# Performance work log

Measured on AMD Instinct MI355X. Metric: run time of the kernel, lower is better.

## Reference

```python
import jax, jax.numpy as jnp
import numpy as np

N_NODES = 50000
N_EDGES = 800000
F_IN = 128
F_OUT = 128


def gcn_conv(x, W, b, src, tgt, w, n):
    # x: [n, F_in]; GCNConv with add_self_loops=True, improved=False (fill=1.0)
    lin = x @ W  # [n, F_out]
    deg = jax.ops.segment_sum(w, tgt, num_segments=n) + 1.0  # self-loop weight 1
    dinv = jax.lax.rsqrt(deg)
    normw = dinv[src] * w * dinv[tgt]  # [E]
    agg = jax.ops.segment_sum(lin[src] * normw[:, None], tgt, num_segments=n)
    return agg + lin * (dinv * dinv)[:, None] + b


def setup_inputs() -> dict:
    key = jax.random.key(0)
    ks = jax.random.split(key, 16)
    X = jax.random.normal(ks[0], (1, N_NODES, F_IN), jnp.float32)
    edge_index = jax.random.randint(ks[1], (2, N_EDGES), 0, N_NODES, jnp.int64)
    edge_weight = jax.random.uniform(ks[2], (N_EDGES,), jnp.float32)
    H = jax.random.normal(ks[3], (1, N_NODES, F_OUT), jnp.float32)
    s = 1.0 / np.sqrt(F_IN)
    s2 = 1.0 / np.sqrt(2 * F_OUT)
    params = {
        'W_z': jax.random.uniform(ks[4], (F_IN, F_OUT), jnp.float32, -s, s),
        'b_z': jnp.zeros((F_OUT,), jnp.float32),
        'W_r': jax.random.uniform(ks[5], (F_IN, F_OUT), jnp.float32, -s, s),
        'b_r': jnp.zeros((F_OUT,), jnp.float32),
        'W_h': jax.random.uniform(ks[6], (F_IN, F_OUT), jnp.float32, -s, s),
        'b_h': jnp.zeros((F_OUT,), jnp.float32),
        'Wl_z': jax.random.uniform(ks[7], (2 * F_OUT, F_OUT), jnp.float32, -s2, s2),
        'bl_z': jax.random.uniform(ks[8], (F_OUT,), jnp.float32, -s2, s2),
        'Wl_r': jax.random.uniform(ks[9], (2 * F_OUT, F_OUT), jnp.float32, -s2, s2),
        'bl_r': jax.random.uniform(ks[10], (F_OUT,), jnp.float32, -s2, s2),
        'Wl_h': jax.random.uniform(ks[11], (2 * F_OUT, F_OUT), jnp.float32, -s2, s2),
        'bl_h': jax.random.uniform(ks[12], (F_OUT,), jnp.float32, -s2, s2),
    }
    return dict(X=X, edge_index=edge_index, edge_weight=edge_weight, H=H, **params)


def reference(X, edge_index, edge_weight, H,
              W_z, b_z, W_r, b_r, W_h, b_h,
              Wl_z, bl_z, Wl_r, bl_r, Wl_h, bl_h):
    B, N, _ = X.shape
    n = B * N
    x = X.reshape(n, -1)
    src, tgt = edge_index[0], edge_index[1]

    cz = gcn_conv(x, W_z, b_z, src, tgt, edge_weight, n).reshape(B, N, -1)
    Z = jax.nn.sigmoid(jnp.concatenate([cz, H], axis=2) @ Wl_z + bl_z)

    cr = gcn_conv(x, W_r, b_r, src, tgt, edge_weight, n).reshape(B, N, -1)
    R = jax.nn.sigmoid(jnp.concatenate([cr, H], axis=2) @ Wl_r + bl_r)

    ch = gcn_conv(x, W_h, b_h, src, tgt, edge_weight, n).reshape(B, N, -1)
    H_tilde = jnp.tanh(jnp.concatenate([ch, H * R], axis=2) @ Wl_h + bl_h)

    return Z * H + (1.0 - Z) * H_tilde
```

## Files before the change

### kernel.cpp

```cpp
#include <hip/hip_runtime.h>
#include <hip/hip_bf16.h>

#define N_NODES 50000
#define N_EDGES 800000
#define M_PAD   50048
#define NBLK5   1564
#define CAP     96

typedef __attribute__((ext_vector_type(8))) short bf16x8_t;
typedef __attribute__((ext_vector_type(4))) float f32x4_t;

__device__ __forceinline__ unsigned short f2bf(float f) {
    unsigned u = __float_as_uint(f);
    u += 0x7FFFu + ((u >> 16) & 1u);
    return (unsigned short)(u >> 16);
}
__device__ __forceinline__ float bf2f(unsigned short h) {
    return __uint_as_float(((unsigned)h) << 16);
}


__global__ void prep1_kernel(const float* __restrict__ Wz, const float* __restrict__ Wr,
                             const float* __restrict__ Wh,
                             const float* __restrict__ bz, const float* __restrict__ br,
                             const float* __restrict__ bh,
                             const float* __restrict__ Wlz, const float* __restrict__ Wlr,
                             const float* __restrict__ Wlh,
                             const float* __restrict__ blz, const float* __restrict__ blr,
                             const float* __restrict__ blh,
                             float* __restrict__ Pf, float* __restrict__ cg,
                             int* __restrict__ counts) {
    int tid = blockIdx.x * 256 + threadIdx.x;
    if (tid < N_NODES) counts[tid] = 0;
    if (tid < 3 * 16384) {
        int g = tid / 16384, k = (tid / 128) % 128, n = tid & 127;
        const float* W  = (g == 0) ? Wz  : (g == 1) ? Wr  : Wh;
        const float* Wl = (g == 0) ? Wlz : (g == 1) ? Wlr : Wlh;
        float acc = 0.f;
        #pragma unroll 8
        for (int j = 0; j < 128; ++j)
            acc = fmaf(W[k * 128 + j], Wl[j * 128 + n], acc);
        Pf[tid] = acc;
    } else if (tid < 3 * 16384 + 384) {
        int u = tid - 3 * 16384;
        int g = u / 128, n = u & 127;
        const float* b  = (g == 0) ? bz  : (g == 1) ? br  : bh;
        const float* Wl = (g == 0) ? Wlz : (g == 1) ? Wlr : Wlh;
        const float* bl = (g == 0) ? blz : (g == 1) ? blr : blh;
        float acc = bl[n];
        #pragma unroll 8
        for (int j = 0; j < 128; ++j)
            acc = fmaf(b[j], Wl[j * 128 + n], acc);
        cg[u] = acc;
    }
}

__global__ void wfrag2_kernel(const float* __restrict__ Pf,
                              const float* __restrict__ Wlz, const float* __restrict__ Wlr,
                              const float* __restrict__ Wlh,
                              unsigned short* __restrict__ Wf2) {
    int tid = blockIdx.x * 256 + threadIdx.x;
    if (tid >= 6 * 2048) return;
    int m = tid / 2048, t = tid % 2048;
    int nt = t / 256, ks = (t / 64) % 4, lane = t % 64;
    const float* src;
    if (m < 3) src = Pf + m * 16384;
    else       src = ((m == 3) ? Wlz : (m == 4) ? Wlr : Wlh) + 128 * 128;
    unsigned short* dst = Wf2 + m * 16384 + ((nt * 4 + ks) * 64 + lane) * 8;
    int n = nt * 16 + (lane & 15);
    int k0 = ks * 32 + 8 * (lane >> 4);
    #pragma unroll
    for (int j = 0; j < 8; ++j) dst[j] = f2bf(src[(k0 + j) * 128 + n]);
}

__global__ void place_kernel(const int* __restrict__ EI, const float* __restrict__ EW,
                             int* __restrict__ counts, int2* __restrict__ rec,
                             const float* __restrict__ Hf, unsigned short* __restrict__ Hb) {
    int i = blockIdx.x * 256 + threadIdx.x;
    if (i < N_NODES * 32) {
        float4 h = ((const float4*)Hf)[i];
        ushort4 b;
        b.x = f2bf(h.x); b.y = f2bf(h.y); b.z = f2bf(h.z); b.w = f2bf(h.w);
        ((ushort4*)Hb)[i] = b;
    }
    if (i < N_EDGES) {
        int s = EI[i];
        int t = EI[N_EDGES + i];
        int pos = atomicAdd(&counts[t], 1);
        if (pos < CAP) rec[(size_t)t * CAP + pos] = make_int2(s, __float_as_int(EW[i]));
    }
}

__global__ void deg_kernel(const int* __restrict__ counts, const int2* __restrict__ rec,
                           float* __restrict__ dinv) {
    int n = blockIdx.x * 256 + threadIdx.x;
    if (n >= N_NODES) return;
    int c = counts[n]; c = (c < CAP) ? c : CAP;
    const int2* rb = rec + (size_t)n * CAP;
    float d = 1.0f;
    #pragma unroll 4
    for (int e = 0; e < c; ++e) d += __int_as_float(rb[e].y);
    dinv[n] = rsqrtf(d);
}

__global__ void convert_kernel(const float* __restrict__ X, const float* __restrict__ dinv,
                               unsigned short* __restrict__ Xb) {
    int i = blockIdx.x * 256 + threadIdx.x;
    if (i >= N_NODES * 32) return;
    int node = i >> 5;
    float di = dinv[node];
    float4 x = ((const float4*)X)[i];
    ushort4 a;
    a.x = f2bf(di * x.x); a.y = f2bf(di * x.y); a.z = f2bf(di * x.z); a.w = f2bf(di * x.w);
    ((ushort4*)Xb)[i] = a;
}


__global__ __launch_bounds__(512) void fused_kernel(const unsigned short* __restrict__ Xb,
                                                    const unsigned short* __restrict__ Hb,
                                                    const float* __restrict__ dinv,
                                                    const int* __restrict__ counts,
                                                    const int2* __restrict__ rec,
                                                    const unsigned short* __restrict__ Wf2,
                                                    const float* __restrict__ cg,
                                                    float* __restrict__ out) {
    __shared__ unsigned short ys[32][136];
    __shared__ unsigned short hs[32][136];
    __shared__ unsigned short rls[32][136];
    int tid = threadIdx.x;
    int wave = tid >> 6, lane = tid & 63;
    int rowbase = blockIdx.x * 32;
    int rlo = lane & 15;
    int kg = 8 * (lane >> 4);
    int n0 = wave;

    {
        int r = tid >> 4, co = (tid & 15) * 8;
        int row = rowbase + r;
        bf16x8_t h;
        if (row < N_NODES) h = *(const bf16x8_t*)(Hb + (size_t)row * 128 + co);
        else {
            #pragma unroll
            for (int j = 0; j < 8; ++j) h[j] = 0;
        }
        *(bf16x8_t*)(&hs[r][co]) = h;
    }

    {
        int nl = wave * 4 + (lane >> 4);
        int half = (lane >> 3) & 1;
        int lg = lane & 7;
        int node = rowbase + nl;
        float acc[16];
        #pragma unroll
        for (int j = 0; j < 16; ++j) acc[j] = 0.f;
        if (node < N_NODES) {
            if (half == 0) {
                bf16x8_t x0 = *(const bf16x8_t*)(Xb + (size_t)node * 128 + lg * 16);
                bf16x8_t x1 = *(const bf16x8_t*)(Xb + (size_t)node * 128 + lg * 16 + 8);
                #pragma unroll
                for (int j = 0; j < 8; ++j) {
                    acc[j] = bf2f((unsigned short)x0[j]);
                    acc[8 + j] = bf2f((unsigned short)x1[j]);
                }
            }
            int c = counts[node]; c = (c < CAP) ? c : CAP;
            const int2* rb = rec + (size_t)node * CAP;
            int e = half;
            int2 r;
            bf16x8_t xa0, xa1;
            float wcur = 0.f;
            if (e < c) {
                r = rb[e];
                xa0 = *(const bf16x8_t*)(Xb + (size_t)r.x * 128 + lg * 16);
                xa1 = *(const bf16x8_t*)(Xb + (size_t)r.x * 128 + lg * 16 + 8);
                wcur = __int_as_float(r.y);
                if (e + 2 < c) r = rb[e + 2];
            }
            while (e < c) {
                bf16x8_t xb0, xb1;
                float wn = 0.f;
                int en = e + 2;
                if (en < c) {
                    xb0 = *(const bf16x8_t*)(Xb + (size_t)r.x * 128 + lg * 16);
                    xb1 = *(const bf16x8_t*)(Xb + (size_t)r.x * 128 + lg * 16 + 8);
                    wn = __int_as_float(r.y);
                    if (en + 2 < c) r = rb[en + 2];
                }
                #pragma unroll
                for (int j = 0; j < 8; ++j) {
                    acc[j] = fmaf(wcur, bf2f((unsigned short)xa0[j]), acc[j]);
                    acc[8 + j] = fmaf(wcur, bf2f((unsigned short)xa1[j]), acc[8 + j]);
                }
                xa0 = xb0; xa1 = xb1; wcur = wn;
                e = en;
            }
        }
        #pragma unroll
        for (int j = 0; j < 16; ++j) acc[j] += __shfl_xor(acc[j], 8, 64);
        if (half == 0) {
            float dt = (node < N_NODES) ? dinv[node] : 0.f;
            ushort4 o0, o1, o2, o3;
            o0.x = f2bf(dt * acc[0]);  o0.y = f2bf(dt * acc[1]);
            o0.z = f2bf(dt * acc[2]);  o0.w = f2bf(dt * acc[3]);
            o1.x = f2bf(dt * acc[4]);  o1.y = f2bf(dt * acc[5]);
            o1.z = f2bf(dt * acc[6]);  o1.w = f2bf(dt * acc[7]);
            o2.x = f2bf(dt * acc[8]);  o2.y = f2bf(dt * acc[9]);
            o2.z = f2bf(dt * acc[10]); o2.w = f2bf(dt * acc[11]);
            o3.x = f2bf(dt * acc[12]); o3.y = f2bf(dt * acc[13]);
            o3.z = f2bf(dt * acc[14]); o3.w = f2bf(dt * acc[15]);
            *(ushort4*)(&ys[nl][lg * 16])      = o0;
            *(ushort4*)(&ys[nl][lg * 16 + 4])  = o1;
            *(ushort4*)(&ys[nl][lg * 16 + 8])  = o2;
            *(ushort4*)(&ys[nl][lg * 16 + 12]) = o3;
        }
    }
    __syncthreads();

    const unsigned short* Az = Wf2;
    const unsigned short* Ar = Wf2 + 16384;
    const unsigned short* Ah = Wf2 + 2 * 16384;
    const unsigned short* Bz = Wf2 + 3 * 16384;
    const unsigned short* Br = Wf2 + 4 * 16384;
    const unsigned short* Bh = Wf2 + 5 * 16384;
    int col = n0 * 16 + rlo;

    {
        f32x4_t a0 = f32x4_t{0.f, 0.f, 0.f, 0.f};
        f32x4_t a1 = f32x4_t{0.f, 0.f, 0.f, 0.f};
        #pragma unroll
        for (int ks = 0; ks < 4; ++ks) {
            bf16x8_t y0 = *(const bf16x8_t*)(&ys[rlo][ks * 32 + kg]);
            bf16x8_t y1 = *(const bf16x8_t*)(&ys[16 + rlo][ks * 32 + kg]);
            bf16x8_t b = *(const bf16x8_t*)(Ar + ((n0 * 4 + ks) * 64 + lane) * 8);
            a0 = __builtin_amdgcn_mfma_f32_16x16x32_bf16(y0, b, a0, 0, 0, 0);
            a1 = __builtin_amdgcn_mfma_f32_16x16x32_bf16(y1, b, a1, 0, 0, 0);
        }
        #pragma unroll
        for (int ks = 0; ks < 4; ++ks) {
            bf16x8_t h0 = *(const bf16x8_t*)(&hs[rlo][ks * 32 + kg]);
            bf16x8_t h1 = *(const bf16x8_t*)(&hs[16 + rlo][ks * 32 + kg]);
            bf16x8_t b = *(const bf16x8_t*)(Br + ((n0 * 4 + ks) * 64 + lane) * 8);
            a0 = __builtin_amdgcn_mfma_f32_16x16x32_bf16(h0, b, a0, 0, 0, 0);
            a1 = __builtin_amdgcn_mfma_f32_16x16x32_bf16(h1, b, a1, 0, 0, 0);
        }
        float crv = cg[128 + col];
        #pragma unroll
        for (int r = 0; r < 4; ++r) {
            float p0 = a0[r] + crv;
            float p1 = a1[r] + crv;
            rls[4 * (lane >> 4) + r][col] = f2bf(1.0f / (1.0f + __expf(-p0)));
            rls[16 + 4 * (lane >> 4) + r][col] = f2bf(1.0f / (1.0f + __expf(-p1)));
        }
    }
    __syncthreads();

    {
        f32x4_t az0 = f32x4_t{0.f, 0.f, 0.f, 0.f};
        f32x4_t az1 = f32x4_t{0.f, 0.f, 0.f, 0.f};
        f32x4_t at0 = f32x4_t{0.f, 0.f, 0.f, 0.f};
        f32x4_t at1 = f32x4_t{0.f, 0.f, 0.f, 0.f};
        #pragma unroll
        for (int ks = 0; ks < 4; ++ks) {
            bf16x8_t y0 = *(const bf16x8_t*)(&ys[rlo][ks * 32 + kg]);
            bf16x8_t y1 = *(const bf16x8_t*)(&ys[16 + rlo][ks * 32 + kg]);
            bf16x8_t bz_ = *(const bf16x8_t*)(Az + ((n0 * 4 + ks) * 64 + lane) * 8);
            bf16x8_t bh_ = *(const bf16x8_t*)(Ah + ((n0 * 4 + ks) * 64 + lane) * 8);
            az0 = __builtin_amdgcn_mfma_f32_16x16x32_bf16(y0, bz_, az0, 0, 0, 0);
            az1 = __builtin_amdgcn_mfma_f32_16x16x32_bf16(y1, bz_, az1, 0, 0, 0);
            at0 = __builtin_amdgcn_mfma_f32_16x16x32_bf16(y0, bh_, at0, 0, 0, 0);
            at1 = __builtin_amdgcn_mfma_f32_16x16x32_bf16(y1, bh_, at1, 0, 0, 0);
        }
        #pragma unroll
        for (int ks = 0; ks < 4; ++ks) {
            bf16x8_t h0 = *(const bf16x8_t*)(&hs[rlo][ks * 32 + kg]);
            bf16x8_t h1 = *(const bf16x8_t*)(&hs[16 + rlo][ks * 32 + kg]);
            bf16x8_t rf0 = *(const bf16x8_t*)(&rls[rlo][ks * 32 + kg]);
            bf16x8_t rf1 = *(const bf16x8_t*)(&rls[16 + rlo][ks * 32 + kg]);
            bf16x8_t hr0, hr1;
            #pragma unroll
            for (int j = 0; j < 8; ++j) {
                hr0[j] = (short)f2bf(bf2f((unsigned short)h0[j]) * bf2f((unsigned short)rf0[j]));
                hr1[j] = (short)f2bf(bf2f((unsigned short)h1[j]) * bf2f((unsigned short)rf1[j]));
            }
            bf16x8_t bz_ = *(const bf16x8_t*)(Bz + ((n0 * 4 + ks) * 64 + lane) * 8);
            bf16x8_t bh_ = *(const bf16x8_t*)(Bh + ((n0 * 4 + ks) * 64 + lane) * 8);
            az0 = __builtin_amdgcn_mfma_f32_16x16x32_bf16(h0, bz_, az0, 0, 0, 0);
            az1 = __builtin_amdgcn_mfma_f32_16x16x32_bf16(h1, bz_, az1, 0, 0, 0);
            at0 = __builtin_amdgcn_mfma_f32_16x16x32_bf16(hr0, bh_, at0, 0, 0, 0);
            at1 = __builtin_amdgcn_mfma_f32_16x16x32_bf16(hr1, bh_, at1, 0, 0, 0);
        }
        float czv = cg[col];
        float chv = cg[256 + col];
        #pragma unroll
        for (int rt = 0; rt < 2; ++rt) {
            #pragma unroll
            for (int r = 0; r < 4; ++r) {
                int rl = rt * 16 + 4 * (lane >> 4) + r;
                int row = rowbase + rl;
                if (row < N_NODES) {
                    float pz = (rt == 0 ? az0[r] : az1[r]) + czv;
                    float z = 1.0f / (1.0f + __expf(-pz));
                    float ph = (rt == 0 ? at0[r] : at1[r]) + chv;
                    float t = __expf(-2.0f * fabsf(ph));
                    float th = (1.0f - t) / (1.0f + t);
                    th = copysignf(th, ph);
                    float h = bf2f(hs[rl][col]);
                    out[(size_t)row * 128 + col] = z * h + (1.0f - z) * th;
                }
            }
        }
    }
}


extern "C" void kernel_launch(void* const* d_in, const int* in_sizes, int n_in,
                              void* d_out, int out_size, void* d_ws, size_t ws_size,
                              hipStream_t stream) {
    const float*      X   = (const float*)d_in[0];
    const int*        EI  = (const int*)d_in[1];
    const float*      EW  = (const float*)d_in[2];
    const float*      Hf  = (const float*)d_in[3];
    const float*      Wz  = (const float*)d_in[4];
    const float*      bz  = (const float*)d_in[5];
    const float*      Wr  = (const float*)d_in[6];
    const float*      br  = (const float*)d_in[7];
    const float*      Wh  = (const float*)d_in[8];
    const float*      bh  = (const float*)d_in[9];
    const float*      Wlz = (const float*)d_in[10];
    const float*      blz = (const float*)d_in[11];
    const float*      Wlr = (const float*)d_in[12];
    const float*      blr = (const float*)d_in[13];
    const float*      Wlh = (const float*)d_in[14];
    const float*      blh = (const float*)d_in[15];
    float* out = (float*)d_out;

    char* p = (char*)d_ws;
    auto alloc = [&](size_t bytes) {
        char* r = p;
        p += (bytes + 255) & ~(size_t)255;
        return r;
    };
    int*   counts = (int*)alloc(M_PAD * 4);
    float* dinv   = (float*)alloc(M_PAD * 4);
    int2*  rec    = (int2*)alloc((size_t)N_NODES * CAP * 8);
    unsigned short* Xb  = (unsigned short*)alloc((size_t)M_PAD * 128 * 2);
    unsigned short* Hb  = (unsigned short*)alloc((size_t)M_PAD * 128 * 2);
    float* Pf  = (float*)alloc(3 * 128 * 128 * 4);
    float* cgb = (float*)alloc(3 * 128 * 4);
    unsigned short* Wf2 = (unsigned short*)alloc(6 * 128 * 128 * 2);

    prep1_kernel<<<196, 256, 0, stream>>>(Wz, Wr, Wh, bz, br, bh,
                                          Wlz, Wlr, Wlh, blz, blr, blh,
                                          Pf, cgb, counts);
    wfrag2_kernel<<<48, 256, 0, stream>>>(Pf, Wlz, Wlr, Wlh, Wf2);
    place_kernel<<<6250, 256, 0, stream>>>(EI, EW, counts, rec, Hf, Hb);
    deg_kernel<<<196, 256, 0, stream>>>(counts, rec, dinv);
    convert_kernel<<<6250, 256, 0, stream>>>(X, dinv, Xb);
    fused_kernel<<<NBLK5, 512, 0, stream>>>(Xb, Hb, dinv, counts, rec, Wf2, cgb, out);
}
```

Measured before the change: 138.3 us.

## Partition edge buckets into four sub-counters and fuse degree with X conversion

Edge placement now spreads atomics across four per-node partition counters (chosen by edge index mod 4), each with its own 24-slot region, to reduce contention on a single counter. The degree and bf16 conversion kernels are merged into one kernel that uses 16 lanes per node for the degree reduction followed by scaling X, which removes a launch and a pass. The aggregation loop walks two partitions per half-wave. The trade-off is a lower per-partition capacity, so edges beyond 24 per partition are dropped even when the node's total is under 96.

```diff
diff --git a/kernel.cpp b/kernel.cpp
--- a/kernel.cpp
+++ b/kernel.cpp
@@ -6,6 +6,9 @@
 #define M_PAD   50048
 #define NBLK5   1564
 #define CAP     96
+#define NPART   4
+#define PCAP    24
+#define CSTRIDE 51200
 
 typedef __attribute__((ext_vector_type(8))) short bf16x8_t;
 typedef __attribute__((ext_vector_type(4))) float f32x4_t;
@@ -31,7 +34,7 @@
                              float* __restrict__ Pf, float* __restrict__ cg,
                              int* __restrict__ counts) {
     int tid = blockIdx.x * 256 + threadIdx.x;
-    if (tid < N_NODES) counts[tid] = 0;
+    if (tid < NPART * CSTRIDE) counts[tid] = 0;
     if (tid < 3 * 16384) {
         int g = tid / 16384, k = (tid / 128) % 128, n = tid & 127;
         const float* W  = (g == 0) ? Wz  : (g == 1) ? Wr  : Wh;
@@ -86,33 +89,42 @@
     if (i < N_EDGES) {
         int s = EI[i];
         int t = EI[N_EDGES + i];
-        int pos = atomicAdd(&counts[t], 1);
-        if (pos < CAP) rec[(size_t)t * CAP + pos] = make_int2(s, __float_as_int(EW[i]));
-    }
-}
-
-__global__ void deg_kernel(const int* __restrict__ counts, const int2* __restrict__ rec,
-                           float* __restrict__ dinv) {
-    int n = blockIdx.x * 256 + threadIdx.x;
-    if (n >= N_NODES) return;
-    int c = counts[n]; c = (c < CAP) ? c : CAP;
-    const int2* rb = rec + (size_t)n * CAP;
-    float d = 1.0f;
-    #pragma unroll 4
-    for (int e = 0; e < c; ++e) d += __int_as_float(rb[e].y);
-    dinv[n] = rsqrtf(d);
-}
-
-__global__ void convert_kernel(const float* __restrict__ X, const float* __restrict__ dinv,
-                               unsigned short* __restrict__ Xb) {
-    int i = blockIdx.x * 256 + threadIdx.x;
-    if (i >= N_NODES * 32) return;
-    int node = i >> 5;
-    float di = dinv[node];
-    float4 x = ((const float4*)X)[i];
-    ushort4 a;
-    a.x = f2bf(di * x.x); a.y = f2bf(di * x.y); a.z = f2bf(di * x.z); a.w = f2bf(di * x.w);
-    ((ushort4*)Xb)[i] = a;
+        int p = i & 3;
+        int pos = atomicAdd(&counts[p * CSTRIDE + t], 1);
+        if (pos < PCAP) rec[(size_t)t * CAP + p * PCAP + pos] = make_int2(s, __float_as_int(EW[i]));
+    }
+}
+
+__global__ void degconv_kernel(const int* __restrict__ counts, const int2* __restrict__ rec,
+                               const float* __restrict__ X,
+                               float* __restrict__ dinv, unsigned short* __restrict__ Xb) {
+    int tid = blockIdx.x * 256 + threadIdx.x;
+    int node = tid >> 4;
+    int j = tid & 15;
+    if (node >= N_NODES) return;
+    const int2* rb = rec + (size_t)node * CAP;
+    float d = 0.f;
+    #pragma unroll
+    for (int p = 0; p < NPART; ++p) {
+        int c = counts[p * CSTRIDE + node]; c = (c < PCAP) ? c : PCAP;
+        for (int e = j; e < c; e += 16) d += __int_as_float(rb[p * PCAP + e].y);
+    }
+    d += __shfl_xor(d, 8, 16);
+    d += __shfl_xor(d, 4, 16);
+    d += __shfl_xor(d, 2, 16);
+    d += __shfl_xor(d, 1, 16);
+    d += 1.0f;
+    float di = rsqrtf(d);
+    if (j == 0) dinv[node] = di;
+    float4 xa = *(const float4*)(X + (size_t)node * 128 + j * 8);
+    float4 xb = *(const float4*)(X + (size_t)node * 128 + j * 8 + 4);
+    ushort4 oa, ob;
+    oa.x = f2bf(di * xa.x); oa.y = f2bf(di * xa.y);
+    oa.z = f2bf(di * xa.z); oa.w = f2bf(di * xa.w);
+    ob.x = f2bf(di * xb.x); ob.y = f2bf(di * xb.y);
+    ob.z = f2bf(di * xb.z); ob.w = f2bf(di * xb.w);
+    *(ushort4*)(Xb + (size_t)node * 128 + j * 8) = oa;
+    *(ushort4*)(Xb + (size_t)node * 128 + j * 8 + 4) = ob;
 }
 
 
@@ -164,36 +176,40 @@
                     acc[8 + j] = bf2f((unsigned short)x1[j]);
                 }
             }
-            int c = counts[node]; c = (c < CAP) ? c : CAP;
-            const int2* rb = rec + (size_t)node * CAP;
-            int e = half;
-            int2 r;
-            bf16x8_t xa0, xa1;
-            float wcur = 0.f;
-            if (e < c) {
-                r = rb[e];
-                xa0 = *(const bf16x8_t*)(Xb + (size_t)r.x * 128 + lg * 16);
-                xa1 = *(const bf16x8_t*)(Xb + (size_t)r.x * 128 + lg * 16 + 8);
-                wcur = __int_as_float(r.y);
-                if (e + 2 < c) r = rb[e + 2];
-            }
-            while (e < c) {
-                bf16x8_t xb0, xb1;
-                float wn = 0.f;
-                int en = e + 2;
-                if (en < c) {
-                    xb0 = *(const bf16x8_t*)(Xb + (size_t)r.x * 128 + lg * 16);
-                    xb1 = *(const bf16x8_t*)(Xb + (size_t)r.x * 128 + lg * 16 + 8);
-                    wn = __int_as_float(r.y);
-                    if (en + 2 < c) r = rb[en + 2];
+            #pragma unroll
+            for (int p2 = 0; p2 < 2; ++p2) {
+                int p = 2 * half + p2;
+                int c = counts[p * CSTRIDE + node]; c = (c < PCAP) ? c : PCAP;
+                const int2* rp = rec + (size_t)node * CAP + p * PCAP;
+                int e = 0;
+                int2 r;
+                bf16x8_t xa0, xa1;
+                float wcur = 0.f;
+                if (e < c) {
+                    r = rp[0];
+                    xa0 = *(const bf16x8_t*)(Xb + (size_t)r.x * 128 + lg * 16);
+                    xa1 = *(const bf16x8_t*)(Xb + (size_t)r.x * 128 + lg * 16 + 8);
+                    wcur = __int_as_float(r.y);
+                    if (1 < c) r = rp[1];
                 }
-                #pragma unroll
-                for (int j = 0; j < 8; ++j) {
-                    acc[j] = fmaf(wcur, bf2f((unsigned short)xa0[j]), acc[j]);
-                    acc[8 + j] = fmaf(wcur, bf2f((unsigned short)xa1[j]), acc[8 + j]);
+                while (e < c) {
+                    bf16x8_t xb0, xb1;
+                    float wn = 0.f;
+                    int en = e + 1;
+                    if (en < c) {
+                        xb0 = *(const bf16x8_t*)(Xb + (size_t)r.x * 128 + lg * 16);
+                        xb1 = *(const bf16x8_t*)(Xb + (size_t)r.x * 128 + lg * 16 + 8);
+                        wn = __int_as_float(r.y);
+                        if (en + 1 < c) r = rp[en + 1];
+                    }
+                    #pragma unroll
+                    for (int j = 0; j < 8; ++j) {
+                        acc[j] = fmaf(wcur, bf2f((unsigned short)xa0[j]), acc[j]);
+                        acc[8 + j] = fmaf(wcur, bf2f((unsigned short)xa1[j]), acc[8 + j]);
+                    }
+                    xa0 = xb0; xa1 = xb1; wcur = wn;
+                    e = en;
                 }
-                xa0 = xb0; xa1 = xb1; wcur = wn;
-                e = en;
             }
         }
         #pragma unroll
@@ -341,7 +357,7 @@
         p += (bytes + 255) & ~(size_t)255;
         return r;
     };
-    int*   counts = (int*)alloc(M_PAD * 4);
+    int*   counts = (int*)alloc((size_t)NPART * CSTRIDE * 4);
     float* dinv   = (float*)alloc(M_PAD * 4);
     int2*  rec    = (int2*)alloc((size_t)N_NODES * CAP * 8);
     unsigned short* Xb  = (unsigned short*)alloc((size_t)M_PAD * 128 * 2);
@@ -350,12 +366,11 @@
     float* cgb = (float*)alloc(3 * 128 * 4);
     unsigned short* Wf2 = (unsigned short*)alloc(6 * 128 * 128 * 2);
 
-    prep1_kernel<<<196, 256, 0, stream>>>(Wz, Wr, Wh, bz, br, bh,
+    prep1_kernel<<<800, 256, 0, stream>>>(Wz, Wr, Wh, bz, br, bh,
                                           Wlz, Wlr, Wlh, blz, blr, blh,
                                           Pf, cgb, counts);
     wfrag2_kernel<<<48, 256, 0, stream>>>(Pf, Wlz, Wlr, Wlh, Wf2);
     place_kernel<<<6250, 256, 0, stream>>>(EI, EW, counts, rec, Hf, Hb);
-    deg_kernel<<<196, 256, 0, stream>>>(counts, rec, dinv);
-    convert_kernel<<<6250, 256, 0, stream>>>(X, dinv, Xb);
+    degconv_kernel<<<3125, 256, 0, stream>>>(counts, rec, X, dinv, Xb);
     fused_kernel<<<NBLK5, 512, 0, stream>>>(Xb, Hb, dinv, counts, rec, Wf2, cgb, out);
 }
```

After: 143.3 us. +3.6%, slower.
